# Performance work log

Hardware: AMD Instinct MI355X
Metric: run time of the kernel (lower is better)

## Reference

```python
import jax, jax.numpy as jnp
import numpy as np

EPS = 1e-5
K_PATCHES = 5000  # sample_pixels // 16


def _resize_bilinear(x, h, w):
    # matches torch F.interpolate(mode='bilinear', align_corners=False)
    return jax.image.resize(x, (x.shape[0], x.shape[1], h, w), method="bilinear", antialias=False)


def _bn(x, g, b, m, v):
    # eval-mode BatchNorm2d with running stats
    inv = jax.lax.rsqrt(v + EPS)
    return (x - m[None, :, None, None]) * (g * inv)[None, :, None, None] + b[None, :, None, None]


def _conv(x, w):
    return jax.lax.conv_general_dilated(x, w, (1, 1), "VALID",
                                        dimension_numbers=("NCHW", "OIHW", "NCHW"))


def setup_inputs():
    key = jax.random.key(0)
    ks = jax.random.split(key, 14)
    B, Hc, Wc = 2, 512, 512
    pha = jax.random.uniform(ks[0], (B, 1, Hc, Wc), jnp.float32)
    err = jax.random.uniform(ks[1], (B, 1, Hc, Wc), jnp.float32)  # strictly >0 so mask is all-ones
    hid = jax.random.normal(ks[2], (B, 32, Hc, Wc), jnp.float32)

    def conv_w(k, o, i):
        return jax.random.normal(k, (o, i, 3, 3), jnp.float32) * 0.05

    def bn_p(k, c):
        k1, k2 = jax.random.split(k)
        return (1.0 + 0.1 * jax.random.normal(k1, (c,), jnp.float32),
                0.1 * jax.random.normal(k2, (c,), jnp.float32),
                jnp.zeros((c,), jnp.float32), jnp.ones((c,), jnp.float32))

    g1, b1, m1, v1 = bn_p(ks[4], 24)
    g2, b2, m2, v2 = bn_p(ks[6], 16)
    g3, b3, m3, v3 = bn_p(ks[8], 12)
    return dict(pha=pha, err=err, hid=hid,
                w1=conv_w(ks[3], 24, 33), g1=g1, b1=b1, m1=m1, v1=v1,
                w2=conv_w(ks[5], 16, 24), g2=g2, b2=b2, m2=m2, v2=v2,
                w3=conv_w(ks[7], 12, 16), g3=g3, b3=b3, m3=m3, v3=v3,
                w4=conv_w(ks[9], 1, 12),
                b4=0.1 * jax.random.normal(ks[10], (1,), jnp.float32),
                H_full=2048, W_full=2048)


def reference(pha, err, hid, w1, g1, b1, m1, v1, w2, g2, b2, m2, v2,
              w3, g3, b3, m3, v3, w4, b4, H_full, W_full):
    B = pha.shape[0]
    Hh, Wh = H_full // 2, W_full // 2
    Hq, Wq = H_full // 4, W_full // 4

    # --- select_refinement_regions (sampling mode) ---
    err_q = _resize_bilinear(err, Hq, Wq)                      # (B,1,Hq,Wq)
    flat = err_q.reshape(B, -1)
    _, top_idx = jax.lax.top_k(flat, K_PATCHES)                # (B,K)
    ref = jnp.zeros_like(flat).at[jnp.arange(B)[:, None], top_idx].set(1.0)
    ref = ref * (flat > 0).astype(flat.dtype)                  # prevent_oversampling
    ref = ref.reshape(B, 1, Hq, Wq)

    # nonzero(ref) == topk locations here (err is strictly positive)
    bidx = jnp.repeat(jnp.arange(B), K_PATCHES)                # (P,)
    hidx = (top_idx // Wq).reshape(-1)                         # (P,)
    widx = (top_idx % Wq).reshape(-1)                          # (P,)

    # --- crop_patch (unfold-equivalent gather), size=2, padding=3 ---
    x = jnp.concatenate([hid, pha], axis=1)                    # (B,33,Hc,Wc)
    x = _resize_bilinear(x, Hh, Wh)                            # (B,33,Hh,Wh)
    pad, size = 3, 2
    win = size + 2 * pad                                       # 8
    xp = jnp.pad(x, ((0, 0), (0, 0), (pad, pad), (pad, pad)))
    rows = hidx[:, None] * size + jnp.arange(win)              # (P,8)
    cols = widx[:, None] * size + jnp.arange(win)              # (P,8)
    patches = xp[bidx[:, None, None], :, rows[:, :, None], cols[:, None, :]]  # (P,8,8,33)
    patches = patches.transpose(0, 3, 1, 2)                    # (P,33,8,8)

    # --- small conv stack ---
    y = jax.nn.relu(_bn(_conv(patches, w1), g1, b1, m1, v1))   # (P,24,6,6)
    y = jax.nn.relu(_bn(_conv(y, w2), g2, b2, m2, v2))         # (P,16,4,4)
    y = jnp.repeat(jnp.repeat(y, 2, axis=2), 2, axis=3)        # nearest -> (P,16,8,8)
    y = jax.nn.relu(_bn(_conv(y, w3), g3, b3, m3, v3))         # (P,12,6,6)
    y = _conv(y, w4) + b4[None, :, None, None]                 # (P,1,4,4)

    # --- replace_patch (scatter_nd of 4x4 blocks into full-res pha) ---
    pha_full = _resize_bilinear(pha, H_full, W_full)           # (B,1,H,W)
    pr = hidx[:, None, None] * 4 + jnp.arange(4)[None, :, None]  # (P,4,1)
    pc = widx[:, None, None] * 4 + jnp.arange(4)[None, None, :]  # (P,1,4)
    pha_full = pha_full.at[bidx[:, None, None], 0, pr, pc].set(y[:, 0])
    return pha_full, ref
```

## Files before the change

### kernel.cpp

```cpp
#include <hip/hip_runtime.h>
#include <stdint.h>

#define K_SEL 5000
#define NQ    262144
#define NB    2

#define BIAS_OFF 38912
#define W4_OFF   39424
#define ST_OFF   40960
#define XT_OFF   131072
#define XT_BYTES ((size_t)NB * NQ * 40 * 2)
#define WS_NEED  (XT_OFF + XT_BYTES)

#define WS_HIST  16
#define WS_SEL   2064
#define WS_EQ    12064
#define EQ_CAP   4096
#define WS_BCNT  20480
#define WS_BBASE 21504

typedef _Float16 f16x8 __attribute__((ext_vector_type(8)));
typedef _Float16 f16x4 __attribute__((ext_vector_type(4)));
typedef float    f32x4 __attribute__((ext_vector_type(4)));
#define MFMA16(a,b,c) __builtin_amdgcn_mfma_f32_16x16x32_f16(a,b,c,0,0,0)

__global__ void prep_kernel(const float* __restrict__ w1, const float* __restrict__ g1,
                            const float* __restrict__ b1, const float* __restrict__ m1,
                            const float* __restrict__ v1,
                            const float* __restrict__ w2, const float* __restrict__ g2,
                            const float* __restrict__ b2, const float* __restrict__ m2,
                            const float* __restrict__ v2,
                            const float* __restrict__ w3, const float* __restrict__ g3,
                            const float* __restrict__ b3, const float* __restrict__ m3,
                            const float* __restrict__ v3,
                            const float* __restrict__ w4, const float* __restrict__ b4,
                            char* __restrict__ ws) {
    _Float16* wf = (_Float16*)ws;
    float* bias = (float*)(ws + BIAS_OFF);
    float* w4r  = (float*)(ws + W4_OFF);
    uint32_t* st = (uint32_t*)(ws + ST_OFF);
    int tid = threadIdx.x;
    for (int t = tid; t < 38 * 512; t += 256) {
        int frag = t >> 9, li = (t >> 3) & 63, j = t & 7;
        int lo = li & 15, hi = li >> 4;
        float val = 0.f;
        if (frag < 18) {
            int ky = frag / 6, r = frag % 6, kx = r >> 1, mt = r & 1;
            int oc = mt * 16 + lo, ci = hi * 8 + j;
            if (oc < 24) val = w1[((oc * 33 + ci) * 3 + ky) * 3 + kx] * g1[oc] * rsqrtf(v1[oc] + 1e-5f);
        } else if (frag < 27) {
            int f = frag - 18, ky = f / 3, kt = f % 3;
            int oc = lo, k = kt * 32 + hi * 8 + j;
            if (k < 72) {
                int kx = k / 24, ci = k % 24;
                val = w2[((oc * 24 + ci) * 3 + ky) * 3 + kx] * g2[oc] * rsqrtf(v2[oc] + 1e-5f);
            }
        } else if (frag < 36) {
            int s = frag - 27, ky = s / 3, kx = s % 3;
            int oc = lo, ci = hi * 8 + j;
            if (oc < 12 && ci < 16) val = w3[((oc * 16 + ci) * 3 + ky) * 3 + kx] * g3[oc] * rsqrtf(v3[oc] + 1e-5f);
        } else {
            int mt = frag - 36, oc = mt * 16 + lo, tap = hi * 8 + j;
            if (oc < 24 && tap < 9)
                val = w1[((oc * 33 + 32) * 3 + tap / 3) * 3 + tap % 3] * g1[oc] * rsqrtf(v1[oc] + 1e-5f);
        }
        wf[t] = (_Float16)val;
    }
    if (tid < 53) {
        float v;
        if (tid < 24)      { float sc = g1[tid] * rsqrtf(v1[tid] + 1e-5f); v = b1[tid] - m1[tid] * sc; }
        else if (tid < 40) { int c = tid - 24; float sc = g2[c] * rsqrtf(v2[c] + 1e-5f); v = b2[c] - m2[c] * sc; }
        else if (tid < 52) { int c = tid - 40; float sc = g3[c] * rsqrtf(v3[c] + 1e-5f); v = b3[c] - m3[c] * sc; }
        else v = b4[0];
        bias[tid] = v;
    }
    if (tid < 144) { int t9 = tid / 16, ci = tid % 16; w4r[tid] = (ci < 12) ? w4[ci * 9 + t9] : 0.f; }
    for (int i = tid; i < WS_HIST + 4 * 512; i += 256) st[i] = 0u;
    __syncthreads();
    if (tid == 0) { st[2] = K_SEL; st[3] = K_SEL; }
}

__global__ void transpose_kernel(const float* __restrict__ hid, const float* __restrict__ pha,
                                 _Float16* __restrict__ xt) {
    int t = blockIdx.x * 256 + threadIdx.x;
    int b = t >> 18, i = t & (NQ - 1);
    _Float16 v[40];
#pragma unroll
    for (int c = 0; c < 32; c++)
        v[c] = (_Float16)hid[((size_t)(b * 32 + c)) * NQ + i];
    v[32] = (_Float16)pha[(size_t)b * NQ + i];
#pragma unroll
    for (int c = 33; c < 40; c++) v[c] = (_Float16)0.f;
    _Float16* dst = xt + (size_t)t * 40;
#pragma unroll
    for (int q = 0; q < 5; q++) *(f16x8*)(dst + q * 8) = *(const f16x8*)(v + q * 8);
}

__global__ void hist_kernel(const float* __restrict__ err, uint32_t* st, int round) {
    __shared__ uint32_t h[256];
    h[threadIdx.x] = 0u;
    __syncthreads();
    int t = blockIdx.x * 256 + threadIdx.x;
    int b = t >> 18;
    uint32_t bits = __float_as_uint(err[t]);
    uint32_t pref = st[b];
    int shift = 24 - 8 * round;
    bool match = (round == 0) || ((bits >> (shift + 8)) == (pref >> (shift + 8)));
    if (match) atomicAdd(&h[(bits >> shift) & 255u], 1u);
    __syncthreads();
    uint32_t v = h[threadIdx.x];
    if (v) atomicAdd(&st[WS_HIST + round * 512 + b * 256 + threadIdx.x], v);
}

__global__ void scan_kernel(uint32_t* st, int round) {
    int b = blockIdx.x;
    int lane = threadIdx.x;
    int shift = 24 - 8 * round;
    const uint32_t* hist = st + WS_HIST + round * 512 + b * 256;
    int binbase = 255 - 4 * lane;
    uint32_t hv0 = hist[binbase], hv1 = hist[binbase - 1],
             hv2 = hist[binbase - 2], hv3 = hist[binbase - 3];
    uint32_t p = hv0 + hv1 + hv2 + hv3;
    uint32_t cum = p;
    for (int o = 1; o < 64; o <<= 1) {
        uint32_t n = __shfl_up(cum, o);
        if (lane >= o) cum += n;
    }
    uint32_t rem = st[2 + b];
    unsigned long long bal = __ballot(cum >= rem);
    int first = __ffsll(bal) - 1;
    if (lane == first) {
        uint32_t acc = cum - p;
        uint32_t hv[4] = {hv0, hv1, hv2, hv3};
        int chosen = binbase;
        for (int q = 0; q < 4; q++) {
            if (acc + hv[q] >= rem) { chosen = binbase - q; break; }
            acc += hv[q];
        }
        uint32_t pref = st[b] | ((uint32_t)chosen << shift);
        st[b] = pref;
        st[2 + b] = rem - acc;
        if (round == 3) { st[4 + b] = pref; st[6 + b] = rem - acc; }
    }
}

__global__ void ccount_kernel(const float* __restrict__ err, uint32_t* st) {
    __shared__ uint32_t wsum[8];
    int blk = blockIdx.x, tid = threadIdx.x;
    int b = blk >> 9, base = (blk & 511) << 9;
    uint32_t T = st[4 + b];
    uint32_t b0 = __float_as_uint(err[b * NQ + base + tid]);
    uint32_t b1 = __float_as_uint(err[b * NQ + base + 256 + tid]);
    unsigned long long m0 = __ballot(b0 > T);
    unsigned long long m1 = __ballot(b1 > T);
    int w = tid >> 6, lane = tid & 63;
    if (lane == 0) { wsum[w] = (uint32_t)__popcll(m0); wsum[4 + w] = (uint32_t)__popcll(m1); }
    __syncthreads();
    if (tid == 0)
        st[WS_BCNT + blk] = wsum[0] + wsum[1] + wsum[2] + wsum[3]
                          + wsum[4] + wsum[5] + wsum[6] + wsum[7];
}

__global__ void cscan_kernel(uint32_t* st) {
    __shared__ uint32_t wtot[8];
    int b = blockIdx.x, tid = threadIdx.x;
    int lane = tid & 63, w = tid >> 6;
    uint32_t v = st[WS_BCNT + b * 512 + tid];
    uint32_t inc = v;
    for (int o = 1; o < 64; o <<= 1) {
        uint32_t n = __shfl_up(inc, o);
        if (lane >= o) inc += n;
    }
    if (lane == 63) wtot[w] = inc;
    __syncthreads();
    uint32_t off = 0;
    for (int j = 0; j < w; j++) off += wtot[j];
    uint32_t base = off + inc - v;
    st[WS_BBASE + b * 512 + tid] = base;
    if (tid == 511) st[8 + b] = base + v;
}

__global__ void cplace_kernel(const float* __restrict__ err, uint32_t* st,
                              float* __restrict__ refout) {
    __shared__ uint32_t wc[8];
    int blk = blockIdx.x, tid = threadIdx.x;
    int b = blk >> 9, base = (blk & 511) << 9;
    uint32_t T = st[4 + b];
    uint32_t blkbase = st[WS_BBASE + b * 512 + (blk & 511)];
    int i0 = base + tid, i1 = base + 256 + tid;
    uint32_t b0 = __float_as_uint(err[b * NQ + i0]);
    uint32_t b1 = __float_as_uint(err[b * NQ + i1]);
    bool s0 = b0 > T, s1 = b1 > T;
    unsigned long long m0 = __ballot(s0);
    unsigned long long m1 = __ballot(s1);
    int w = tid >> 6, lane = tid & 63;
    if (lane == 0) { wc[w] = (uint32_t)__popcll(m0); wc[4 + w] = (uint32_t)__popcll(m1); }
    refout[b * NQ + i0] = s0 ? 1.0f : 0.0f;
    refout[b * NQ + i1] = s1 ? 1.0f : 0.0f;
    __syncthreads();
    uint32_t tot0 = wc[0] + wc[1] + wc[2] + wc[3];
    uint32_t pre0 = 0, pre1 = tot0;
    for (int j = 0; j < w; j++) { pre0 += wc[j]; pre1 += wc[4 + j]; }
    unsigned long long lt = (1ull << lane) - 1ull;
    if (s0) {
        uint32_t slot = blkbase + pre0 + (uint32_t)__popcll(m0 & lt);
        if (slot < K_SEL) st[WS_SEL + b * K_SEL + slot] = (uint32_t)i0;
    }
    if (s1) {
        uint32_t slot = blkbase + pre1 + (uint32_t)__popcll(m1 & lt);
        if (slot < K_SEL) st[WS_SEL + b * K_SEL + slot] = (uint32_t)i1;
    }
    if (b0 == T) { uint32_t e = atomicAdd(&st[10 + b], 1u); if (e < EQ_CAP) st[WS_EQ + b * EQ_CAP + e] = (uint32_t)i0; }
    if (b1 == T) { uint32_t e = atomicAdd(&st[10 + b], 1u); if (e < EQ_CAP) st[WS_EQ + b * EQ_CAP + e] = (uint32_t)i1; }
}

__global__ void select_kernel(uint32_t* st, float* __restrict__ refout) {
    __shared__ uint32_t L[EQ_CAP];
    int b = blockIdx.x;
    uint32_t m = st[10 + b]; if (m > EQ_CAP) m = EQ_CAP;
    uint32_t need = st[6 + b];
    uint32_t T = st[4 + b];
    for (uint32_t j = threadIdx.x; j < m; j += blockDim.x) L[j] = st[WS_EQ + b * EQ_CAP + j];
    __syncthreads();
    for (uint32_t j = threadIdx.x; j < m; j += blockDim.x) {
        uint32_t idx = L[j];
        uint32_t rank = 0;
        for (uint32_t q = 0; q < m; q++) rank += (L[q] < idx) ? 1u : 0u;
        if (rank < need) {
            uint32_t slot = atomicAdd(&st[8 + b], 1u);
            if (slot < K_SEL) st[WS_SEL + b * K_SEL + slot] = idx;
            refout[b * NQ + idx] = (T != 0u) ? 1.0f : 0.0f;
        }
    }
}

__global__ void upsample_kernel(const float* __restrict__ pha, float* __restrict__ out) {
    int t = blockIdx.x * 256 + threadIdx.x;
    int xq = t & 511;
    int rest = t >> 9;
    int oy = rest & 2047;
    int b  = rest >> 11;
    const float* src = pha + (size_t)b * NQ;
    float sy = oy * 0.25f - 0.375f;
    sy = fminf(fmaxf(sy, 0.0f), 511.0f);
    int y0 = (int)sy; int y1i = min(y0 + 1, 511);
    float fy = sy - (float)y0;
    float rv[4];
#pragma unroll
    for (int j = 0; j < 4; j++) {
        int ox = xq * 4 + j;
        float sx = ox * 0.25f - 0.375f;
        sx = fminf(fmaxf(sx, 0.0f), 511.0f);
        int x0 = (int)sx; int x1i = min(x0 + 1, 511);
        float fx = sx - (float)x0;
        float v00 = src[y0 * 512 + x0],  v01 = src[y0 * 512 + x1i];
        float v10 = src[y1i * 512 + x0], v11 = src[y1i * 512 + x1i];
        rv[j] = v00 * (1.f - fy) * (1.f - fx) + v01 * (1.f - fy) * fx
              + v10 * fy * (1.f - fx)         + v11 * fy * fx;
    }
    float4 r4 = make_float4(rv[0], rv[1], rv[2], rv[3]);
    *reinterpret_cast<float4*>(out + (size_t)b * 4194304 + (size_t)oy * 2048 + xq * 4) = r4;
}

__device__ __forceinline__ f16x8 ldfrag(const _Float16* wf, int frag, int l) {
    return *(const f16x8*)(wf + frag * 512 + l * 8);
}

template<bool XT>
__global__ __launch_bounds__(128) void patch_kernel(
    const float* __restrict__ hid, const float* __restrict__ pha,
    const _Float16* __restrict__ xt,
    const char* __restrict__ ws, float* __restrict__ out) {
    __shared__ _Float16 xs[64][40];
    __shared__ _Float16 y1n[36][40];
    __shared__ _Float16 pool[64][40];
    __shared__ float pha8[64];
    __shared__ float biasL[56];
    float* y3s = (float*)&y1n[0][0];

    const _Float16* wf = (const _Float16*)ws;
    const float* biasG = (const float*)(ws + BIAS_OFF);
    const float* w4r   = (const float*)(ws + W4_OFF);
    const uint32_t* st = (const uint32_t*)(ws + ST_OFF);

    int tid = threadIdx.x, l = tid & 63, wid = tid >> 6;
    int lo = l & 15, hi = l >> 4;
    int bp = blockIdx.x;
    int b = (bp >= K_SEL) ? 1 : 0;
    int pi = bp - b * K_SEL;
    uint32_t idx = st[WS_SEL + b * K_SEL + pi] & 0x3FFFFu;
    int hq = (int)(idx >> 9), wq = (int)(idx & 511u);

    if (tid < 53) biasL[tid] = biasG[tid];

    int ry = l >> 3, rx = l & 7;
    int hy = hq * 2 + ry - 3, hx = wq * 2 + rx - 3;
    bool inb = ((unsigned)hy < 1024u) && ((unsigned)hx < 1024u);
    float sy = fminf(fmaxf(hy * 0.5f - 0.25f, 0.f), 511.f);
    float sx = fminf(fmaxf(hx * 0.5f - 0.25f, 0.f), 511.f);
    int y0 = (int)sy, x0 = (int)sx;
    int y1c = min(y0 + 1, 511), x1c = min(x0 + 1, 511);
    float fy = sy - (float)y0, fx = sx - (float)x0;
    int o00 = y0 * 512 + x0, o01 = y0 * 512 + x1c, o10 = y1c * 512 + x0, o11 = y1c * 512 + x1c;
    float w00 = (1.f - fy) * (1.f - fx), w01 = (1.f - fy) * fx;
    float w10 = fy * (1.f - fx), w11 = fy * fx;

    _Float16 hv[16];
    if (XT) {
        if (inb) {
            const _Float16* xtb = xt + (size_t)b * NQ * 40 + (size_t)wid * 16;
            const _Float16* p00 = xtb + (size_t)o00 * 40;
            const _Float16* p01 = xtb + (size_t)o01 * 40;
            const _Float16* p10 = xtb + (size_t)o10 * 40;
            const _Float16* p11 = xtb + (size_t)o11 * 40;
            f16x8 a0 = *(const f16x8*)p00, a1 = *(const f16x8*)(p00 + 8);
            f16x8 b0 = *(const f16x8*)p01, b1 = *(const f16x8*)(p01 + 8);
            f16x8 c0 = *(const f16x8*)p10, c1 = *(const f16x8*)(p10 + 8);
            f16x8 d0 = *(const f16x8*)p11, d1 = *(const f16x8*)(p11 + 8);
#pragma unroll
            for (int j = 0; j < 8; j++) {
                hv[j]     = (_Float16)(w00 * (float)a0[j] + w01 * (float)b0[j]
                                     + w10 * (float)c0[j] + w11 * (float)d0[j]);
                hv[j + 8] = (_Float16)(w00 * (float)a1[j] + w01 * (float)b1[j]
                                     + w10 * (float)c1[j] + w11 * (float)d1[j]);
            }
        } else {
#pragma unroll
            for (int c = 0; c < 16; c++) hv[c] = (_Float16)0.f;
        }
    } else {
        const float* hb = hid + ((size_t)b * 32 + wid * 16) * NQ;
#pragma unroll
        for (int c = 0; c < 16; c++) {
            const float* p = hb + (size_t)c * NQ;
            float v = 0.f;
            if (inb) v = p[o00] * w00 + p[o01] * w01 + p[o10] * w10 + p[o11] * w11;
            hv[c] = (_Float16)v;
        }
    }
    f16x8 h0 = {hv[0], hv[1], hv[2], hv[3], hv[4], hv[5], hv[6], hv[7]};
    f16x8 h1 = {hv[8], hv[9], hv[10], hv[11], hv[12], hv[13], hv[14], hv[15]};
    {
        _Float16* xrow = &xs[l][wid * 16];
        *(f16x8*)xrow = h0;
        *((f16x8*)xrow + 1) = h1;
    }
    f16x8 z8 = {(_Float16)0.f, (_Float16)0.f, (_Float16)0.f, (_Float16)0.f,
                (_Float16)0.f, (_Float16)0.f, (_Float16)0.f, (_Float16)0.f};
    if (wid == 1) {
        const float* p = pha + (size_t)b * NQ;
        float v = 0.f;
        if (inb) v = p[o00] * w00 + p[o01] * w01 + p[o10] * w10 + p[o11] * w11;
        pha8[l] = v;
    }
    __syncthreads();

    if (wid == 0) {
        if (l < 48) {
            int py = (l * 43) >> 8, px = l - py * 6;
            _Float16 tap[9];
#pragma unroll
            for (int t = 0; t < 9; t++) {
                int ky = t / 3, kx = t % 3;
                int ip = (py + ky) * 8 + px + kx;
                tap[t] = (_Float16)pha8[ip & 63];
            }
            _Float16* row = &pool[l][0];
            f16x8 r0 = {tap[0], tap[1], tap[2], tap[3], tap[4], tap[5], tap[6], tap[7]};
            f16x8 r1 = z8; r1[0] = tap[8];
            *(f16x8*)row = r0;
            *(f16x8*)(row + 8)  = r1;
            *(f16x8*)(row + 16) = z8;
            *(f16x8*)(row + 24) = z8;
        }
    } else {
        for (int i = l; i < 72; i += 64) {
            *(f16x8*)&y1n[i >> 1][24 + (i & 1) * 8] = z8;
        }
    }
    __syncthreads();

    f32x4 zf = {0.f, 0.f, 0.f, 0.f};
    f32x4 aA0 = zf, aA1 = zf, aB = zf;
    int nA = wid * 16 + lo, nB = 32 + lo;
    int pyA = (nA * 43) >> 8, pxA = nA - pyA * 6;
    int pyB = (nB * 43) >> 8, pxB = nB - pyB * 6;
    {
        f16x8 A0 = ldfrag(wf, 36, l), A1 = ldfrag(wf, 37, l);
        f16x8 BA = *(const f16x8*)&pool[nA][hi * 8];
        f16x8 BB = *(const f16x8*)&pool[nB][hi * 8];
        aA0 = MFMA16(A0, BA, aA0);
        aA1 = MFMA16(A1, BA, aA1);
        aB  = MFMA16(wid ? A1 : A0, BB, aB);
    }
#pragma unroll
    for (int ky = 0; ky < 3; ky++) {
#pragma unroll
        for (int kt = 0; kt < 3; kt++) {
            f16x8 A0 = ldfrag(wf, ky * 6 + kt * 2 + 0, l);
            f16x8 A1 = ldfrag(wf, ky * 6 + kt * 2 + 1, l);
            int rA = ((pyA + ky) * 8 + pxA + kt) & 63;
            int rB = ((pyB + ky) * 8 + pxB + kt) & 63;
            f16x8 BA = *(const f16x8*)&xs[rA][hi * 8];
            f16x8 BB = *(const f16x8*)&xs[rB][hi * 8];
            aA0 = MFMA16(A0, BA, aA0);
            aA1 = MFMA16(A1, BA, aA1);
            aB  = MFMA16(wid ? A1 : A0, BB, aB);
        }
    }
    {
        f32x4 accs[3] = {aA0, aA1, aB};
        int mts[3] = {0, 1, wid};
        int nts[3] = {wid, wid, 2};
#pragma unroll
        for (int f = 0; f < 3; f++) {
            int n = nts[f] * 16 + lo;
            int ocb = mts[f] * 16 + hi * 4;
            if (n < 36 && ocb < 24) {
                f16x4 hh;
                hh[0] = (_Float16)fmaxf(accs[f][0] + biasL[ocb + 0], 0.f);
                hh[1] = (_Float16)fmaxf(accs[f][1] + biasL[ocb + 1], 0.f);
                hh[2] = (_Float16)fmaxf(accs[f][2] + biasL[ocb + 2], 0.f);
                hh[3] = (_Float16)fmaxf(accs[f][3] + biasL[ocb + 3], 0.f);
                *(f16x4*)&y1n[n][ocb] = hh;
            }
        }
    }
    __syncthreads();

    if (wid == 0) {
        f32x4 a2 = zf;
        int qy = lo >> 2, qx = lo & 3;
#pragma unroll
        for (int ky = 0; ky < 3; ky++) {
#pragma unroll
            for (int kt = 0; kt < 3; kt++) {
                f16x8 A = ldfrag(wf, 18 + ky * 3 + kt, l);
                int k = kt * 32 + hi * 8;
                const _Float16* bptr;
                if (k < 72) {
                    int kx = k / 24, ci0 = k - kx * 24;
                    bptr = &y1n[(qy + ky) * 6 + qx + kx][ci0];
                } else {
                    bptr = &y1n[0][24];
                }
                f16x8 B = *(const f16x8*)bptr;
                a2 = MFMA16(A, B, a2);
            }
        }
        int ocb = hi * 4;
        f16x4 hh;
        hh[0] = (_Float16)fmaxf(a2[0] + biasL[24 + ocb + 0], 0.f);
        hh[1] = (_Float16)fmaxf(a2[1] + biasL[24 + ocb + 1], 0.f);
        hh[2] = (_Float16)fmaxf(a2[2] + biasL[24 + ocb + 2], 0.f);
        hh[3] = (_Float16)fmaxf(a2[3] + biasL[24 + ocb + 3], 0.f);
#pragma unroll
        for (int dy = 0; dy < 2; dy++)
#pragma unroll
            for (int dx = 0; dx < 2; dx++) {
                int row = (2 * qy + dy) * 8 + 2 * qx + dx;
                *(f16x4*)&pool[row][ocb] = hh;
            }
    } else {
        *(f16x8*)&pool[l][16] = z8;
        *(f16x8*)&pool[l][24] = z8;
    }
    __syncthreads();

    f32x4 aC = zf, aD = zf;
    int nC = wid * 16 + lo, nD = 32 + lo;
    int pyC = (nC * 43) >> 8, pxC = nC - pyC * 6;
    int pyD = (nD * 43) >> 8, pxD = nD - pyD * 6;
#pragma unroll
    for (int s = 0; s < 9; s++) {
        int ky = s / 3, kx = s % 3;
        f16x8 A = ldfrag(wf, 27 + s, l);
        f16x8 BC = *(const f16x8*)&pool[((pyC + ky) * 8 + pxC + kx) & 63][hi * 8];
        aC = MFMA16(A, BC, aC);
        if (wid) {
            f16x8 BD = *(const f16x8*)&pool[((pyD + ky) * 8 + pxD + kx) & 63][hi * 8];
            aD = MFMA16(A, BD, aD);
        }
    }
    __syncthreads();
    {
        int ocb = hi * 4;
        f32x4 accs[2] = {aC, aD};
        int nts[2] = {wid, 2};
        int cnt = wid ? 2 : 1;
        for (int f = 0; f < cnt; f++) {
            int n = nts[f] * 16 + lo;
            if (n < 36) {
                f32x4 v;
#pragma unroll
                for (int r = 0; r < 4; r++) {
                    float bb = (ocb + r < 12) ? biasL[40 + ocb + r] : 0.f;
                    float x = accs[f][r] + bb;
                    v[r] = (ocb + r < 12) ? fmaxf(x, 0.f) : 0.f;
                }
                *(f32x4*)&y3s[n * 16 + ocb] = v;
            }
        }
    }
    __syncthreads();

    if (wid == 0) {
        int r4 = lo >> 2, c4 = lo & 3, cig = hi;
        float acc = 0.f;
#pragma unroll
        for (int t = 0; t < 9; t++) {
            int ky = t / 3, kx = t % 3;
            const f32x4 xv = *(const f32x4*)&y3s[((r4 + ky) * 6 + c4 + kx) * 16 + cig * 4];
            const f32x4 wv = *(const f32x4*)(w4r + t * 16 + cig * 4);
            acc += xv[0] * wv[0] + xv[1] * wv[1] + xv[2] * wv[2] + xv[3] * wv[3];
        }
        acc += __shfl_xor(acc, 32);
        acc += __shfl_xor(acc, 16);
        if (l < 16) {
            out[(size_t)b * 4194304 + (size_t)(hq * 4 + r4) * 2048 + (wq * 4 + c4)] = acc + biasL[52];
        }
    }
}

extern "C" void kernel_launch(void* const* d_in, const int* in_sizes, int n_in,
                              void* d_out, int out_size, void* d_ws, size_t ws_size,
                              hipStream_t stream) {
    const float* pha = (const float*)d_in[0];
    const float* err = (const float*)d_in[1];
    const float* hid = (const float*)d_in[2];
    const float* w1  = (const float*)d_in[3];
    const float* g1  = (const float*)d_in[4];
    const float* bb1 = (const float*)d_in[5];
    const float* m1  = (const float*)d_in[6];
    const float* v1  = (const float*)d_in[7];
    const float* w2  = (const float*)d_in[8];
    const float* g2  = (const float*)d_in[9];
    const float* bb2 = (const float*)d_in[10];
    const float* m2  = (const float*)d_in[11];
    const float* v2  = (const float*)d_in[12];
    const float* w3  = (const float*)d_in[13];
    const float* g3  = (const float*)d_in[14];
    const float* bb3 = (const float*)d_in[15];
    const float* m3  = (const float*)d_in[16];
    const float* v3  = (const float*)d_in[17];
    const float* w4  = (const float*)d_in[18];
    const float* b4  = (const float*)d_in[19];

    float* out    = (float*)d_out;
    float* refout = out + (size_t)NB * 4194304;
    char* ws      = (char*)d_ws;
    uint32_t* st  = (uint32_t*)(ws + ST_OFF);
    _Float16* xt  = (_Float16*)(ws + XT_OFF);
    bool use_xt   = (ws_size >= WS_NEED);

    prep_kernel<<<1, 256, 0, stream>>>(w1, g1, bb1, m1, v1, w2, g2, bb2, m2, v2,
                                       w3, g3, bb3, m3, v3, w4, b4, ws);
    if (use_xt)
        transpose_kernel<<<2048, 256, 0, stream>>>(hid, pha, xt);
    for (int r = 0; r < 4; r++) {
        hist_kernel<<<2048, 256, 0, stream>>>(err, st, r);
        scan_kernel<<<2, 64, 0, stream>>>(st, r);
    }
    ccount_kernel<<<1024, 256, 0, stream>>>(err, st);
    cscan_kernel<<<2, 512, 0, stream>>>(st);
    cplace_kernel<<<1024, 256, 0, stream>>>(err, st, refout);
    select_kernel<<<2, 256, 0, stream>>>(st, refout);
    upsample_kernel<<<8192, 256, 0, stream>>>(pha, out);
    if (use_xt)
        patch_kernel<true><<<2 * K_SEL, 128, 0, stream>>>(hid, pha, xt, ws, out);
    else
        patch_kernel<false><<<2 * K_SEL, 128, 0, stream>>>(hid, pha, xt, ws, out);
}
```

Before: 156.3 us.

## Piggyback transpose and upsample blocks onto radix-select kernel launches

```diff
diff --git a/kernel.cpp b/kernel.cpp
--- a/kernel.cpp
+++ b/kernel.cpp
@@ -8,7 +8,7 @@
 #define BIAS_OFF 38912
 #define W4_OFF   39424
 #define ST_OFF   40960
-#define XT_OFF   131072
+#define XT_OFF   135168
 #define XT_BYTES ((size_t)NB * NQ * 40 * 2)
 #define WS_NEED  (XT_OFF + XT_BYTES)
 
@@ -80,23 +80,85 @@
     if (tid == 0) { st[2] = K_SEL; st[3] = K_SEL; }
 }
 
-__global__ void transpose_kernel(const float* __restrict__ hid, const float* __restrict__ pha,
-                                 _Float16* __restrict__ xt) {
+__device__ __forceinline__ void tu_work(int tb, const float* __restrict__ hid,
+                                        const float* __restrict__ pha,
+                                        _Float16* __restrict__ xt,
+                                        float* __restrict__ out) {
+    int tid = threadIdx.x;
+    if (tb < 2048) {
+        int t = tb * 256 + tid;
+        int b = t >> 18, i = t & (NQ - 1);
+        _Float16 v[40];
+#pragma unroll
+        for (int c = 0; c < 32; c++)
+            v[c] = (_Float16)hid[((size_t)(b * 32 + c)) * NQ + i];
+        v[32] = (_Float16)pha[(size_t)b * NQ + i];
+#pragma unroll
+        for (int c = 33; c < 40; c++) v[c] = (_Float16)0.f;
+        _Float16* dst = xt + (size_t)t * 40;
+#pragma unroll
+        for (int q = 0; q < 5; q++) *(f16x8*)(dst + q * 8) = *(const f16x8*)(v + q * 8);
+    } else {
+        int t = (tb - 2048) * 256 + tid;
+        int xq = t & 511;
+        int rest = t >> 9;
+        int oy = rest & 2047;
+        int b  = rest >> 11;
+        const float* src = pha + (size_t)b * NQ;
+        float sy = oy * 0.25f - 0.375f;
+        sy = fminf(fmaxf(sy, 0.0f), 511.0f);
+        int y0 = (int)sy; int y1i = min(y0 + 1, 511);
+        float fy = sy - (float)y0;
+        float rv[4];
+#pragma unroll
+        for (int j = 0; j < 4; j++) {
+            int ox = xq * 4 + j;
+            float sx = ox * 0.25f - 0.375f;
+            sx = fminf(fmaxf(sx, 0.0f), 511.0f);
+            int x0 = (int)sx; int x1i = min(x0 + 1, 511);
+            float fx = sx - (float)x0;
+            float v00 = src[y0 * 512 + x0],  v01 = src[y0 * 512 + x1i];
+            float v10 = src[y1i * 512 + x0], v11 = src[y1i * 512 + x1i];
+            rv[j] = v00 * (1.f - fy) * (1.f - fx) + v01 * (1.f - fy) * fx
+                  + v10 * fy * (1.f - fx)         + v11 * fy * fx;
+        }
+        float4 r4 = make_float4(rv[0], rv[1], rv[2], rv[3]);
+        *reinterpret_cast<float4*>(out + (size_t)b * 4194304 + (size_t)oy * 2048 + xq * 4) = r4;
+    }
+}
+
+__global__ void upsample_kernel(const float* __restrict__ pha, float* __restrict__ out) {
     int t = blockIdx.x * 256 + threadIdx.x;
-    int b = t >> 18, i = t & (NQ - 1);
-    _Float16 v[40];
-#pragma unroll
-    for (int c = 0; c < 32; c++)
-        v[c] = (_Float16)hid[((size_t)(b * 32 + c)) * NQ + i];
-    v[32] = (_Float16)pha[(size_t)b * NQ + i];
-#pragma unroll
-    for (int c = 33; c < 40; c++) v[c] = (_Float16)0.f;
-    _Float16* dst = xt + (size_t)t * 40;
-#pragma unroll
-    for (int q = 0; q < 5; q++) *(f16x8*)(dst + q * 8) = *(const f16x8*)(v + q * 8);
-}
-
-__global__ void hist_kernel(const float* __restrict__ err, uint32_t* st, int round) {
+    int xq = t & 511;
+    int rest = t >> 9;
+    int oy = rest & 2047;
+    int b  = rest >> 11;
+    const float* src = pha + (size_t)b * NQ;
+    float sy = oy * 0.25f - 0.375f;
+    sy = fminf(fmaxf(sy, 0.0f), 511.0f);
+    int y0 = (int)sy; int y1i = min(y0 + 1, 511);
+    float fy = sy - (float)y0;
+    float rv[4];
+#pragma unroll
+    for (int j = 0; j < 4; j++) {
+        int ox = xq * 4 + j;
+        float sx = ox * 0.25f - 0.375f;
+        sx = fminf(fmaxf(sx, 0.0f), 511.0f);
+        int x0 = (int)sx; int x1i = min(x0 + 1, 511);
+        float fx = sx - (float)x0;
+        float v00 = src[y0 * 512 + x0],  v01 = src[y0 * 512 + x1i];
+        float v10 = src[y1i * 512 + x0], v11 = src[y1i * 512 + x1i];
+        rv[j] = v00 * (1.f - fy) * (1.f - fx) + v01 * (1.f - fy) * fx
+              + v10 * fy * (1.f - fx)         + v11 * fy * fx;
+    }
+    float4 r4 = make_float4(rv[0], rv[1], rv[2], rv[3]);
+    *reinterpret_cast<float4*>(out + (size_t)b * 4194304 + (size_t)oy * 2048 + xq * 4) = r4;
+}
+
+__global__ void hist_kernel(const float* __restrict__ err, uint32_t* st, int round,
+                            const float* __restrict__ hid, const float* __restrict__ pha,
+                            _Float16* __restrict__ xt, float* __restrict__ out, int tu_base) {
+    if (blockIdx.x >= 2048) { tu_work(blockIdx.x - 2048 + tu_base, hid, pha, xt, out); return; }
     __shared__ uint32_t h[256];
     h[threadIdx.x] = 0u;
     __syncthreads();
@@ -144,7 +206,10 @@
     }
 }
 
-__global__ void ccount_kernel(const float* __restrict__ err, uint32_t* st) {
+__global__ void ccount_kernel(const float* __restrict__ err, uint32_t* st,
+                              const float* __restrict__ hid, const float* __restrict__ pha,
+                              _Float16* __restrict__ xt, float* __restrict__ out, int tu_base) {
+    if (blockIdx.x >= 1024) { tu_work(blockIdx.x - 1024 + tu_base, hid, pha, xt, out); return; }
     __shared__ uint32_t wsum[8];
     int blk = blockIdx.x, tid = threadIdx.x;
     int b = blk >> 9, base = (blk & 511) << 9;
@@ -181,7 +246,10 @@
 }
 
 __global__ void cplace_kernel(const float* __restrict__ err, uint32_t* st,
-                              float* __restrict__ refout) {
+                              float* __restrict__ refout,
+                              const float* __restrict__ hid, const float* __restrict__ pha,
+                              _Float16* __restrict__ xt, float* __restrict__ out, int tu_base) {
+    if (blockIdx.x >= 1024) { tu_work(blockIdx.x - 1024 + tu_base, hid, pha, xt, out); return; }
     __shared__ uint32_t wc[8];
     int blk = blockIdx.x, tid = threadIdx.x;
     int b = blk >> 9, base = (blk & 511) << 9;
@@ -232,34 +300,6 @@
             refout[b * NQ + idx] = (T != 0u) ? 1.0f : 0.0f;
         }
     }
-}
-
-__global__ void upsample_kernel(const float* __restrict__ pha, float* __restrict__ out) {
-    int t = blockIdx.x * 256 + threadIdx.x;
-    int xq = t & 511;
-    int rest = t >> 9;
-    int oy = rest & 2047;
-    int b  = rest >> 11;
-    const float* src = pha + (size_t)b * NQ;
-    float sy = oy * 0.25f - 0.375f;
-    sy = fminf(fmaxf(sy, 0.0f), 511.0f);
-    int y0 = (int)sy; int y1i = min(y0 + 1, 511);
-    float fy = sy - (float)y0;
-    float rv[4];
-#pragma unroll
-    for (int j = 0; j < 4; j++) {
-        int ox = xq * 4 + j;
-        float sx = ox * 0.25f - 0.375f;
-        sx = fminf(fmaxf(sx, 0.0f), 511.0f);
-        int x0 = (int)sx; int x1i = min(x0 + 1, 511);
-        float fx = sx - (float)x0;
-        float v00 = src[y0 * 512 + x0],  v01 = src[y0 * 512 + x1i];
-        float v10 = src[y1i * 512 + x0], v11 = src[y1i * 512 + x1i];
-        rv[j] = v00 * (1.f - fy) * (1.f - fx) + v01 * (1.f - fy) * fx
-              + v10 * fy * (1.f - fx)         + v11 * fy * fx;
-    }
-    float4 r4 = make_float4(rv[0], rv[1], rv[2], rv[3]);
-    *reinterpret_cast<float4*>(out + (size_t)b * 4194304 + (size_t)oy * 2048 + xq * 4) = r4;
 }
 
 __device__ __forceinline__ f16x8 ldfrag(const _Float16* wf, int frag, int l) {
@@ -555,19 +595,37 @@
 
     prep_kernel<<<1, 256, 0, stream>>>(w1, g1, bb1, m1, v1, w2, g2, bb2, m2, v2,
                                        w3, g3, bb3, m3, v3, w4, b4, ws);
-    if (use_xt)
-        transpose_kernel<<<2048, 256, 0, stream>>>(hid, pha, xt);
-    for (int r = 0; r < 4; r++) {
-        hist_kernel<<<2048, 256, 0, stream>>>(err, st, r);
-        scan_kernel<<<2, 64, 0, stream>>>(st, r);
-    }
-    ccount_kernel<<<1024, 256, 0, stream>>>(err, st);
-    cscan_kernel<<<2, 512, 0, stream>>>(st);
-    cplace_kernel<<<1024, 256, 0, stream>>>(err, st, refout);
-    select_kernel<<<2, 256, 0, stream>>>(st, refout);
-    upsample_kernel<<<8192, 256, 0, stream>>>(pha, out);
-    if (use_xt)
+    if (use_xt) {
+        const int NTU = 10240, SLICE = 1707;
+        int off = 0;
+        for (int r = 0; r < 4; r++) {
+            int n = (off + SLICE <= NTU) ? SLICE : (NTU - off);
+            hist_kernel<<<2048 + n, 256, 0, stream>>>(err, st, r, hid, pha, xt, out, off);
+            off += n;
+            scan_kernel<<<2, 64, 0, stream>>>(st, r);
+        }
+        {
+            int n = (off + SLICE <= NTU) ? SLICE : (NTU - off);
+            ccount_kernel<<<1024 + n, 256, 0, stream>>>(err, st, hid, pha, xt, out, off);
+            off += n;
+        }
+        cscan_kernel<<<2, 512, 0, stream>>>(st);
+        {
+            int n = NTU - off;
+            cplace_kernel<<<1024 + n, 256, 0, stream>>>(err, st, refout, hid, pha, xt, out, off);
+        }
+        select_kernel<<<2, 256, 0, stream>>>(st, refout);
         patch_kernel<true><<<2 * K_SEL, 128, 0, stream>>>(hid, pha, xt, ws, out);
-    else
+    } else {
+        upsample_kernel<<<8192, 256, 0, stream>>>(pha, out);
+        for (int r = 0; r < 4; r++) {
+            hist_kernel<<<2048, 256, 0, stream>>>(err, st, r, hid, pha, xt, out, 0);
+            scan_kernel<<<2, 64, 0, stream>>>(st, r);
+        }
+        ccount_kernel<<<1024, 256, 0, stream>>>(err, st, hid, pha, xt, out, 0);
+        cscan_kernel<<<2, 512, 0, stream>>>(st);
+        cplace_kernel<<<1024, 256, 0, stream>>>(err, st, refout, hid, pha, xt, out, 0);
+        select_kernel<<<2, 256, 0, stream>>>(st, refout);
         patch_kernel<false><<<2 * K_SEL, 128, 0, stream>>>(hid, pha, xt, ws, out);
-}
+    }
+}
```

Result: faster. 152.7 us (-2.3%).
